# Kernel optimization log

Measured on AMD Instinct MI355X. Metric: run time of the kernel, lower is better.

## Reference

```python
import jax, jax.numpy as jnp
import numpy as np

B, S, HID = 8, 1024, 1024
NH, HD = 16, 64  # num heads, head dim; NH*HD == HID


def setup_inputs() -> dict:
    key = jax.random.key(0)
    ks = jax.random.split(key, 8)
    sc = 0.02
    return {
        "hidden_states": jax.random.normal(ks[0], (B, S, HID), jnp.float32),
        "attention_mask": jnp.zeros((B, 1, 1, S), jnp.float32),
        "Wq": jax.random.normal(ks[1], (HID, HID), jnp.float32) * sc,
        "bq": jnp.zeros((HID,), jnp.float32),
        "Wk": jax.random.normal(ks[2], (HID, HID), jnp.float32) * sc,
        "bk": jnp.zeros((HID,), jnp.float32),
        "Wv": jax.random.normal(ks[3], (HID, HID), jnp.float32) * sc,
        "bv": jnp.zeros((HID,), jnp.float32),
    }


def reference(hidden_states, attention_mask, Wq, bq, Wk, bk, Wv, bv):
    def split_heads(x):  # [B,S,HID] -> [B,NH,S,HD]
        return x.reshape(B, S, NH, HD).transpose(0, 2, 1, 3)

    q = split_heads(hidden_states @ Wq + bq)
    k = split_heads(hidden_states @ Wk + bk)
    v = split_heads(hidden_states @ Wv + bv)

    # [B,NH,S,S] score matrix, scale, additive mask, softmax
    scores = jnp.einsum("bhqd,bhkd->bhqk", q, k) / jnp.sqrt(jnp.float32(HD))
    scores = scores + attention_mask
    probs = jax.nn.softmax(scores, axis=-1)  # dropout prob = 0.0 -> identity

    ctx = jnp.einsum("bhqk,bhkd->bhqd", probs, v)
    return ctx.transpose(0, 2, 1, 3).reshape(B, S, HID)
```

## Files before the change

kernel.cpp:

```cpp
#include <hip/hip_runtime.h>


typedef __bf16 bf16x8 __attribute__((ext_vector_type(8)));
typedef float f32x4 __attribute__((ext_vector_type(4)));
typedef float f32x16 __attribute__((ext_vector_type(16)));
typedef int i32x4 __attribute__((ext_vector_type(4)));

__device__ __forceinline__ unsigned rne16(float x) {
  unsigned u = __builtin_bit_cast(unsigned, x);
  return (u + 0x7fffu + ((u >> 16) & 1u)) >> 16;
}
__device__ __forceinline__ unsigned packbf(float lo, float hi) {
  return rne16(lo) | (rne16(hi) << 16);
}
__device__ __forceinline__ unsigned packbf_fast(float lo, float hi) {
  unsigned ul = __builtin_bit_cast(unsigned, lo) + 0x8000u;
  unsigned uh = __builtin_bit_cast(unsigned, hi) + 0x8000u;
  return __builtin_amdgcn_perm(uh, ul, 0x07060302u);
}
__device__ __forceinline__ void async16(void* l, const void* g) {
  __builtin_amdgcn_global_load_lds((const __attribute__((address_space(1))) void*)g,
                                   (__attribute__((address_space(3))) void*)l, 16, 0, 0);
}
__device__ __forceinline__ bf16x8 dsr128(const char* p) {
  i32x4 r;
  unsigned a = (unsigned)(size_t)(const __attribute__((address_space(3))) char*)p;
  asm volatile("ds_read_b128 %0, %1" : "=v"(r) : "v"(a));
  return __builtin_bit_cast(bf16x8, r);
}

__global__ __launch_bounds__(256) void k_prep(const float* __restrict__ h,
                                              unsigned short* __restrict__ hbf,
                                              const float* __restrict__ Wq,
                                              const float* __restrict__ Wk,
                                              const float* __restrict__ Wv,
                                              unsigned short* __restrict__ wt) {
  __shared__ float t[32][33];
  int bid = blockIdx.x, tid = threadIdx.x;
  if (bid < 8192) {
    size_t i = (size_t)bid * 256 + tid;
    float4 v = ((const float4*)h)[i];
    uint2 r;
    r.x = packbf(v.x, v.y);
    r.y = packbf(v.z, v.w);
    ((uint2*)hbf)[i] = r;
  } else {
    int id = bid - 8192;
    int which = id >> 10;
    int sub = id & 1023;
    int c0 = (sub & 31) * 32, k0 = (sub >> 5) * 32;
    const float* W = which == 0 ? Wq : (which == 1 ? Wk : Wv);
    int tx = tid & 31, ty = tid >> 5;
#pragma unroll
    for (int i = 0; i < 4; ++i) {
      int r = ty + i * 8;
      t[r][tx] = W[(size_t)(k0 + r) * 1024 + c0 + tx];
    }
    __syncthreads();
#pragma unroll
    for (int i = 0; i < 4; ++i) {
      int r = ty + i * 8;
      wt[((size_t)which * 1024 + c0 + r) * 1024 + k0 + tx] = (unsigned short)rne16(t[tx][r]);
    }
  }
}

__global__ __launch_bounds__(512, 2) void k_gemm(const unsigned short* __restrict__ A,
                                                 const unsigned short* __restrict__ Bm,
                                                 const float* __restrict__ bq,
                                                 const float* __restrict__ bk,
                                                 const float* __restrict__ bv,
                                                 unsigned short* __restrict__ qkv,
                                                 unsigned short* __restrict__ vt) {
  __shared__ __align__(16) char lds[98304];
  const int tid = threadIdx.x;
  const int w = tid >> 6, lane = tid & 63;
  const int wm = w >> 1, wn = w & 1;

  int orig = blockIdx.x;
  int wgid = (orig & 7) * 96 + (orig >> 3);
  int tm = wgid / 24, tn = wgid - tm * 24;
  int m0 = tm * 256, n0 = tn * 128;

  int ro[2], ke[2];
#pragma unroll
  for (int j = 0; j < 2; ++j) {
    int o = j * 8192 + tid * 16;
    int s = o >> 10, w10 = o & 1023;
    int lg = w10 ^ (((w10 >> 9) & 1) << 5);
    ro[j] = ((s >> 1) << 4) + (lg >> 6);
    ke[j] = ((s & 1) << 5) + ((lg & 63) >> 1);
  }
  auto stage_half = [&](int ldsoff, const unsigned short* src, int rb, int k0) {
#pragma unroll
    for (int j = 0; j < 2; ++j)
      async16(lds + ldsoff + j * 8192 + w * 1024,
              src + (size_t)(rb + ro[j]) * 1024 + (k0 + ke[j]));
  };
  auto stA = [&](int t) {
    int d = (t & 1) * 49152;
    stage_half(d, A, m0, t * 64);
    stage_half(d + 16384, A, m0 + 128, t * 64);
  };
  auto stB = [&](int t) { stage_half((t & 1) * 49152 + 32768, Bm, n0, t * 64); };

  const int lswz = (((lane & 15) << 6) | ((lane >> 4) << 4)) ^ ((lane & 8) << 2);

  f32x4 acc[4][4];
#pragma unroll
  for (int i = 0; i < 4; ++i)
#pragma unroll
    for (int j = 0; j < 4; ++j)
#pragma unroll
      for (int e = 0; e < 4; ++e) acc[i][j][e] = 0.f;

  stA(0); stB(0); stB(1);
  asm volatile("s_waitcnt vmcnt(2)");
  __builtin_amdgcn_s_barrier();
  __builtin_amdgcn_sched_barrier(0);

#pragma unroll 1
  for (int it = 0; it < 8; ++it) {
    const int u = it * 2;
    const bool pf = it < 7;
#pragma unroll
    for (int G = 0; G < 2; ++G) {
      const char* abase = lds + G * 49152 + (wm >> 1) * 16384 + lswz;
      const char* bbase = lds + G * 49152 + 32768 + lswz;
      bf16x8 bF[4][2];
#pragma unroll
      for (int ph = 0; ph < 2; ++ph) {
        if (ph == 0) {
#pragma unroll
          for (int n = 0; n < 4; ++n)
#pragma unroll
            for (int ks = 0; ks < 2; ++ks)
              bF[n][ks] = dsr128(bbase + ((wn * 4 + n) * 2 + ks) * 1024);
        }
        bf16x8 aF[2][2];
#pragma unroll
        for (int mm = 0; mm < 2; ++mm)
#pragma unroll
          for (int ks = 0; ks < 2; ++ks)
            aF[mm][ks] =
                dsr128(abase + (((wm & 1) * 4 + ph * 2 + mm) * 2 + ks) * 1024);
        if (G == 0) {
          if (ph == 0) stA(u + 1);
          else if (pf) stB(u + 2);
        } else {
          if (ph == 0) { if (pf) stA(u + 2); }
          else if (pf) stB(u + 3);
        }
        __builtin_amdgcn_s_barrier();
        asm volatile("s_waitcnt lgkmcnt(0)");
        __builtin_amdgcn_sched_barrier(0);
        __builtin_amdgcn_s_setprio(1);
#pragma unroll
        for (int ks = 0; ks < 2; ++ks)
#pragma unroll
          for (int mm = 0; mm < 2; ++mm)
#pragma unroll
            for (int n = 0; n < 4; ++n)
              acc[ph * 2 + mm][n] = __builtin_amdgcn_mfma_f32_16x16x32_bf16(
                  aF[mm][ks], bF[n][ks], acc[ph * 2 + mm][n], 0, 0, 0);
        __builtin_amdgcn_s_setprio(0);
        if (ph == 1) {
          if (G == 0) {
            if (pf) asm volatile("s_waitcnt vmcnt(2)");
            else    asm volatile("s_waitcnt vmcnt(0)");
          } else {
            if (pf) asm volatile("s_waitcnt vmcnt(2)");
          }
        }
        __builtin_amdgcn_s_barrier();
        __builtin_amdgcn_sched_barrier(0);
      }
    }
  }

  const int which = tn >> 3;
  const int ng = n0 & 1023;
  const int b = m0 >> 10;
  const int r = lane & 15, qq = lane >> 4;
  const int sb = (m0 & 1023) + wm * 64 + qq * 4;

  if (which != 2) {
    const float* bp = which == 0 ? bq : bk;
    unsigned short* base = qkv + ((size_t)which << 23) + ((size_t)b << 20);
#pragma unroll
    for (int n = 0; n < 4; ++n) {
      int n_in = ng + wn * 64 + n * 16 + r;
      float bias = bp[n_in];
      unsigned short* dp = base + ((size_t)(n_in >> 6) << 16) + (n_in & 63);
#pragma unroll
      for (int m = 0; m < 4; ++m)
#pragma unroll
        for (int e = 0; e < 4; ++e)
          dp[(size_t)(sb + m * 16 + e) << 6] = (unsigned short)rne16(acc[m][n][e] + bias);
    }
  } else {
    unsigned short* vbase = vt + ((size_t)b << 20);
#pragma unroll
    for (int n = 0; n < 4; ++n) {
      int n_in = ng + wn * 64 + n * 16 + r;
      float bias = bv[n_in];
      unsigned short* dp = vbase + ((size_t)n_in << 10) + sb;
#pragma unroll
      for (int m = 0; m < 4; ++m) {
        uint2 pk;
        pk.x = packbf(acc[m][n][0] + bias, acc[m][n][1] + bias);
        pk.y = packbf(acc[m][n][2] + bias, acc[m][n][3] + bias);
        *(uint2*)(dp + m * 16) = pk;
      }
    }
  }
}

__global__ __launch_bounds__(256, 4) void k_attn(const unsigned short* __restrict__ qg,
                                                 const unsigned short* __restrict__ kg,
                                                 const unsigned short* __restrict__ vtg,
                                                 const float* __restrict__ maskg,
                                                 float* __restrict__ out) {
  __shared__ __align__(16) char lds[36864];
  char* KF = lds;
  char* VF = lds + 16384;
  float* MK = (float*)(lds + 32768);
  int tid = threadIdx.x, w = tid >> 6, lane = tid & 63, l5 = lane & 31, q5 = lane >> 5;
  int idx = blockIdx.x;
  int bi = idx & 7;
  int j = idx >> 3;
  int h = j >> 3, qc = j & 7;
  int bh = bi * 16 + h, s0 = qc * 128;
  const unsigned short* qb = qg + ((size_t)bh << 16);
  const unsigned short* kb = kg + ((size_t)bh << 16);
  const unsigned short* vb = vtg + ((size_t)bh << 16);
  const float LG = 1.4426950408889634f;
  const float C1 = 0.125f * LG;

  {
    float4 mv = *(const float4*)(maskg + (size_t)bi * 1024 + tid * 4);
    mv.x *= LG; mv.y *= LG; mv.z *= LG; mv.w *= LG;
    *(float4*)(MK + tid * 4) = mv;
  }

  bf16x8 qfr[4];
#pragma unroll
  for (int ds = 0; ds < 4; ++ds)
    qfr[ds] = *(const bf16x8*)(qb + (size_t)(s0 + w * 32 + l5) * 64 + ds * 16 + q5 * 8);

  f32x16 O[2];
#pragma unroll
  for (int i = 0; i < 2; ++i)
#pragma unroll
    for (int e = 0; e < 16; ++e) O[i][e] = 0.f;
  float lsum = 0.f;

#pragma unroll 1
  for (int kt = 0; kt < 8; ++kt) {
    int k0 = kt * 128;
    __syncthreads();
#pragma unroll
    for (int t = 0; t < 4; ++t) {
      int f = w * 4 + t, mt = f >> 2, ds = f & 3;
      async16(KF + f * 1024, kb + (size_t)(k0 + mt * 32 + l5) * 64 + ds * 16 + q5 * 8);
    }
#pragma unroll
    for (int t = 0; t < 4; ++t) {
      int f = w * 4 + t, dt = f >> 3, ks = f & 7;
      async16(VF + f * 1024, vb + (size_t)(dt * 32 + l5) * 1024 + k0 + ks * 16 + q5 * 8);
    }
    __syncthreads();

#pragma unroll
    for (int mt = 0; mt < 4; ++mt) {
      f32x16 S;
#pragma unroll
      for (int e = 0; e < 16; ++e) S[e] = 0.f;
#pragma unroll
      for (int ds = 0; ds < 4; ++ds) {
        bf16x8 a = *(const bf16x8*)(KF + (mt * 4 + ds) * 1024 + lane * 16);
        S = __builtin_amdgcn_mfma_f32_32x32x16_bf16(a, qfr[ds], S, 0, 0, 0);
      }
      float p[16];
#pragma unroll
      for (int g4 = 0; g4 < 4; ++g4) {
        float4 mv = *(const float4*)(MK + k0 + mt * 32 + g4 * 8 + q5 * 4);
        p[g4 * 4 + 0] = __builtin_amdgcn_exp2f(S[g4 * 4 + 0] * C1 + mv.x);
        p[g4 * 4 + 1] = __builtin_amdgcn_exp2f(S[g4 * 4 + 1] * C1 + mv.y);
        p[g4 * 4 + 2] = __builtin_amdgcn_exp2f(S[g4 * 4 + 2] * C1 + mv.z);
        p[g4 * 4 + 3] = __builtin_amdgcn_exp2f(S[g4 * 4 + 3] * C1 + mv.w);
      }
      unsigned p2[8];
#pragma unroll
      for (int e = 0; e < 16; ++e) lsum += p[e];
#pragma unroll
      for (int jj = 0; jj < 8; ++jj) p2[jj] = packbf_fast(p[2 * jj], p[2 * jj + 1]);
#pragma unroll
      for (int kh = 0; kh < 2; ++kh) {
        int ks = mt * 2 + kh, gp = kh * 4;
        bf16x8 av0 = *(const bf16x8*)(VF + (0 * 8 + ks) * 1024 + lane * 16);
        bf16x8 av1 = *(const bf16x8*)(VF + (1 * 8 + ks) * 1024 + lane * 16);
        unsigned o0 = p2[gp + 0], o1 = p2[gp + 1];
        unsigned o2 = p2[gp + 2], o3 = p2[gp + 3];
        unsigned t0 = __shfl_xor((int)o0, 32);
        unsigned t1 = __shfl_xor((int)o1, 32);
        unsigned t2 = __shfl_xor((int)o2, 32);
        unsigned t3 = __shfl_xor((int)o3, 32);
        uint4 fu;
        fu.x = q5 ? t2 : o0;
        fu.y = q5 ? t3 : o1;
        fu.z = q5 ? o2 : t0;
        fu.w = q5 ? o3 : t1;
        bf16x8 bfrag = __builtin_bit_cast(bf16x8, fu);
        O[0] = __builtin_amdgcn_mfma_f32_32x32x16_bf16(av0, bfrag, O[0], 0, 0, 0);
        O[1] = __builtin_amdgcn_mfma_f32_32x32x16_bf16(av1, bfrag, O[1], 0, 0, 0);
      }
    }
  }

  __syncthreads();
  float* Ob = (float*)(lds + w * 8192);
  float lt = lsum + __shfl_xor(lsum, 32);
  float rinv = 1.0f / lt;
#pragma unroll
  for (int dt = 0; dt < 2; ++dt)
#pragma unroll
    for (int g4 = 0; g4 < 4; ++g4) {
      float4 val;
      val.x = O[dt][g4 * 4 + 0] * rinv;
      val.y = O[dt][g4 * 4 + 1] * rinv;
      val.z = O[dt][g4 * 4 + 2] * rinv;
      val.w = O[dt][g4 * 4 + 3] * rinv;
      int c = dt * 8 + g4 * 2 + q5;
      *(float4*)(Ob + l5 * 64 + (c ^ (l5 & 15)) * 4) = val;
    }
#pragma unroll
  for (int t = 0; t < 8; ++t) {
    int qr = t * 4 + (lane >> 4), cr = lane & 15;
    float4 vv = *(const float4*)(Ob + qr * 64 + (cr ^ (qr & 15)) * 4);
    int s = s0 + w * 32 + qr;
    *(float4*)(out + (((size_t)(bi * 1024 + s)) << 10) + (h << 6) + (cr << 2)) = vv;
  }
}

extern "C" void kernel_launch(void* const* d_in, const int* in_sizes, int n_in,
                              void* d_out, int out_size, void* d_ws, size_t ws_size,
                              hipStream_t stream) {
  (void)in_sizes; (void)n_in; (void)out_size; (void)ws_size;
  const float* hidden = (const float*)d_in[0];
  const float* mask = (const float*)d_in[1];
  const float* Wq = (const float*)d_in[2];
  const float* bq = (const float*)d_in[3];
  const float* Wk = (const float*)d_in[4];
  const float* bk = (const float*)d_in[5];
  const float* Wv = (const float*)d_in[6];
  const float* bv = (const float*)d_in[7];
  float* out = (float*)d_out;
  char* ws = (char*)d_ws;
  unsigned short* hbf = (unsigned short*)ws;
  unsigned short* wt  = (unsigned short*)(ws + 16777216);
  unsigned short* qkv = (unsigned short*)(ws + 23068672);
  unsigned short* vt  = (unsigned short*)(ws + 56623104);

  k_prep<<<11264, 256, 0, stream>>>(hidden, hbf, Wq, Wk, Wv, wt);
  k_gemm<<<768, 512, 0, stream>>>(hbf, wt, bq, bk, bv, qkv, vt);
  k_attn<<<1024, 256, 0, stream>>>(qkv, qkv + 8388608, vt, mask, out);
}
```

Baseline: 218.7 us.

## Triple-buffer QKV GEMM LDS pipeline with one barrier per k-tile

Replaces the two-buffer QKV projection main loop, which staged A and B on separate schedules with two barriers per half-step, with a three-stage LDS ring (144 KB). Each k-tile is prefetched two iterations ahead, and one barrier per tile replaces the previous four per pair of tiles. MFMA over the first k-half overlaps the LDS reads of the second half via a partial lgkmcnt wait. The goal is to cut barrier stalls and hide global-load latency, at the cost of much more LDS, which likely drops occupancy from two workgroups per CU to one despite launch_bounds(512,2).

After: 215.7 us. No clear change (-1.4%).

```diff
diff --git a/kernel.cpp b/kernel.cpp
--- a/kernel.cpp
+++ b/kernel.cpp
@@ -72,7 +72,7 @@
                                                  const float* __restrict__ bv,
                                                  unsigned short* __restrict__ qkv,
                                                  unsigned short* __restrict__ vt) {
-  __shared__ __align__(16) char lds[98304];
+  __shared__ __align__(16) char lds[147456];
   const int tid = threadIdx.x;
   const int w = tid >> 6, lane = tid & 63;
   const int wm = w >> 1, wn = w & 1;
@@ -97,12 +97,11 @@
       async16(lds + ldsoff + j * 8192 + w * 1024,
               src + (size_t)(rb + ro[j]) * 1024 + (k0 + ke[j]));
   };
-  auto stA = [&](int t) {
-    int d = (t & 1) * 49152;
-    stage_half(d, A, m0, t * 64);
-    stage_half(d + 16384, A, m0 + 128, t * 64);
+  auto stAB = [&](int t, int doff) {
+    stage_half(doff, A, m0, t * 64);
+    stage_half(doff + 16384, A, m0 + 128, t * 64);
+    stage_half(doff + 32768, Bm, n0, t * 64);
   };
-  auto stB = [&](int t) { stage_half((t & 1) * 49152 + 32768, Bm, n0, t * 64); };
 
   const int lswz = (((lane & 15) << 6) | ((lane >> 4) << 4)) ^ ((lane & 8) << 2);
 
@@ -114,68 +113,60 @@
 #pragma unroll
       for (int e = 0; e < 4; ++e) acc[i][j][e] = 0.f;
 
-  stA(0); stB(0); stB(1);
-  asm volatile("s_waitcnt vmcnt(2)");
+  stAB(0, 0);
+  stAB(1, 49152);
+  asm volatile("s_waitcnt vmcnt(6)");
   __builtin_amdgcn_s_barrier();
   __builtin_amdgcn_sched_barrier(0);
 
+  int cur = 0;
 #pragma unroll 1
-  for (int it = 0; it < 8; ++it) {
-    const int u = it * 2;
-    const bool pf = it < 7;
-#pragma unroll
-    for (int G = 0; G < 2; ++G) {
-      const char* abase = lds + G * 49152 + (wm >> 1) * 16384 + lswz;
-      const char* bbase = lds + G * 49152 + 32768 + lswz;
-      bf16x8 bF[4][2];
-#pragma unroll
-      for (int ph = 0; ph < 2; ++ph) {
-        if (ph == 0) {
-#pragma unroll
-          for (int n = 0; n < 4; ++n)
-#pragma unroll
-            for (int ks = 0; ks < 2; ++ks)
-              bF[n][ks] = dsr128(bbase + ((wn * 4 + n) * 2 + ks) * 1024);
-        }
-        bf16x8 aF[2][2];
-#pragma unroll
-        for (int mm = 0; mm < 2; ++mm)
-#pragma unroll
-          for (int ks = 0; ks < 2; ++ks)
-            aF[mm][ks] =
-                dsr128(abase + (((wm & 1) * 4 + ph * 2 + mm) * 2 + ks) * 1024);
-        if (G == 0) {
-          if (ph == 0) stA(u + 1);
-          else if (pf) stB(u + 2);
-        } else {
-          if (ph == 0) { if (pf) stA(u + 2); }
-          else if (pf) stB(u + 3);
-        }
-        __builtin_amdgcn_s_barrier();
-        asm volatile("s_waitcnt lgkmcnt(0)");
-        __builtin_amdgcn_sched_barrier(0);
-        __builtin_amdgcn_s_setprio(1);
-#pragma unroll
-        for (int ks = 0; ks < 2; ++ks)
-#pragma unroll
-          for (int mm = 0; mm < 2; ++mm)
-#pragma unroll
-            for (int n = 0; n < 4; ++n)
-              acc[ph * 2 + mm][n] = __builtin_amdgcn_mfma_f32_16x16x32_bf16(
-                  aF[mm][ks], bF[n][ks], acc[ph * 2 + mm][n], 0, 0, 0);
-        __builtin_amdgcn_s_setprio(0);
-        if (ph == 1) {
-          if (G == 0) {
-            if (pf) asm volatile("s_waitcnt vmcnt(2)");
-            else    asm volatile("s_waitcnt vmcnt(0)");
-          } else {
-            if (pf) asm volatile("s_waitcnt vmcnt(2)");
-          }
-        }
-        __builtin_amdgcn_s_barrier();
-        __builtin_amdgcn_sched_barrier(0);
-      }
-    }
+  for (int kt = 0; kt < 16; ++kt) {
+    const char* buf = lds + cur * 49152;
+    int nxt2 = cur + 2; if (nxt2 >= 3) nxt2 -= 3;
+    const char* abase = buf + (wm >> 1) * 16384 + lswz;
+    const char* bbase = buf + 32768 + lswz;
+    bf16x8 aF[4][2], bF[4][2];
+#pragma unroll
+    for (int n = 0; n < 4; ++n)
+      bF[n][0] = dsr128(bbase + ((wn * 4 + n) * 2 + 0) * 1024);
+#pragma unroll
+    for (int mt = 0; mt < 4; ++mt)
+      aF[mt][0] = dsr128(abase + (((wm & 1) * 4 + mt) * 2 + 0) * 1024);
+    if (kt < 14) stAB(kt + 2, nxt2 * 49152);
+#pragma unroll
+    for (int n = 0; n < 4; ++n)
+      bF[n][1] = dsr128(bbase + ((wn * 4 + n) * 2 + 1) * 1024);
+#pragma unroll
+    for (int mt = 0; mt < 4; ++mt)
+      aF[mt][1] = dsr128(abase + (((wm & 1) * 4 + mt) * 2 + 1) * 1024);
+    asm volatile("s_waitcnt lgkmcnt(8)");
+    __builtin_amdgcn_sched_barrier(0);
+    __builtin_amdgcn_s_setprio(1);
+#pragma unroll
+    for (int mt = 0; mt < 4; ++mt)
+#pragma unroll
+      for (int n = 0; n < 4; ++n)
+        acc[mt][n] = __builtin_amdgcn_mfma_f32_16x16x32_bf16(aF[mt][0], bF[n][0],
+                                                             acc[mt][n], 0, 0, 0);
+    __builtin_amdgcn_s_setprio(0);
+    asm volatile("s_waitcnt lgkmcnt(0)");
+    __builtin_amdgcn_sched_barrier(0);
+    __builtin_amdgcn_s_setprio(1);
+#pragma unroll
+    for (int mt = 0; mt < 4; ++mt)
+#pragma unroll
+      for (int n = 0; n < 4; ++n)
+        acc[mt][n] = __builtin_amdgcn_mfma_f32_16x16x32_bf16(aF[mt][1], bF[n][1],
+                                                             acc[mt][n], 0, 0, 0);
+    __builtin_amdgcn_s_setprio(0);
+    if (kt < 14) asm volatile("s_waitcnt vmcnt(6)");
+    else if (kt == 14) asm volatile("s_waitcnt vmcnt(0)");
+    if (kt < 15) {
+      __builtin_amdgcn_s_barrier();
+      __builtin_amdgcn_sched_barrier(0);
+    }
+    cur = cur + 1; if (cur == 3) cur = 0;
   }
 
   const int which = tn >> 3;
```
